# Kernel tuning notes

Hardware: AMD Instinct MI355X
Metric: run time of the kernel (lower is better)

The kernel has to match this reference:

```python
import jax, jax.numpy as jnp
import numpy as np

N_QUBITS = 14
LATENT = 14
DEPTH = 4
BATCH = 256
DIM = 1 << N_QUBITS  # 16384 amplitudes

# PennyLane convention: wire 0 is the most-significant bit of the flat state index.
_idx = np.arange(DIM)
_bits = (_idx[None, :] >> (N_QUBITS - 1 - np.arange(N_QUBITS)[:, None])) & 1  # [n_qubits, DIM]
_parity = np.sum(_bits[:-1] * _bits[1:], axis=0) % 2  # adjacent-pair CZ chain parity
CZ_SIGNS = jnp.asarray(1.0 - 2.0 * _parity, dtype=jnp.complex64)  # [DIM]
Z_SIGNS = jnp.asarray(1 - 2 * _bits[:LATENT], dtype=jnp.float32)  # [LATENT, DIM]


def _rx(t):
    c = jnp.cos(0.5 * t) + 0j
    s = -1j * jnp.sin(0.5 * t)
    m = jnp.stack([jnp.stack([c, s], -1), jnp.stack([s, c], -1)], -2)
    return m.astype(jnp.complex64)


def _ry(t):
    c = jnp.cos(0.5 * t)
    s = jnp.sin(0.5 * t)
    m = jnp.stack([jnp.stack([c, -s], -1), jnp.stack([s, c], -1)], -2)
    return m.astype(jnp.complex64)


def _rz(t):
    e = jnp.exp(-0.5j * t.astype(jnp.complex64))
    z = jnp.zeros_like(e)
    m = jnp.stack([jnp.stack([e, z], -1), jnp.stack([z, jnp.conj(e)], -1)], -2)
    return m.astype(jnp.complex64)


def _apply_1q(state, mat, wire):
    # state: [B, DIM]; mat: [2,2] (shared) or [B,2,2] (per-sample)
    B = state.shape[0]
    left = 1 << wire
    right = 1 << (N_QUBITS - wire - 1)
    st = state.reshape(B, left, 2, right)
    if mat.ndim == 3:
        st = jnp.einsum('bij,bajc->baic', mat, st)
    else:
        st = jnp.einsum('ij,bajc->baic', mat, st)
    return st.reshape(B, DIM)


def setup_inputs() -> dict:
    key = jax.random.key(0)
    k1, k2, k3, k4 = jax.random.split(key, 4)
    conditioning = jax.random.normal(k1, (BATCH, LATENT), dtype=jnp.float32)
    lim = 1.0 / np.sqrt(LATENT)
    W_enc = jax.random.uniform(k2, (N_QUBITS, LATENT), jnp.float32, -lim, lim)
    b_enc = jax.random.uniform(k3, (N_QUBITS,), jnp.float32, -lim, lim)
    # TorchLayer default init: U(0, 2*pi)
    weights = jax.random.uniform(k4, (DEPTH, N_QUBITS, 3), jnp.float32, 0.0, 2.0 * np.pi)
    return {"conditioning": conditioning, "W_enc": W_enc, "b_enc": b_enc, "weights": weights}


def reference(conditioning, W_enc, b_enc, weights):
    # encode: Linear + SiLU -> per-wire rotation angles [B, n_qubits]
    emb = conditioning @ W_enc.T + b_enc
    emb = emb * jax.nn.sigmoid(emb)
    B = emb.shape[0]

    state = jnp.zeros((B, DIM), jnp.complex64).at[:, 0].set(1.0)

    # angle encoding: RX(v) then RY(v) on each wire (per-sample gates)
    for w in range(N_QUBITS):
        v = emb[:, w]
        U = jnp.einsum('bij,bjk->bik', _ry(v), _rx(v))  # [B,2,2]
        state = _apply_1q(state, U, w)

    # variational layers: RZ, RX, RY per wire (shared gates), then CZ chain
    for d in range(DEPTH):
        for w in range(N_QUBITS):
            p = weights[d, w]
            U = _ry(p[2]) @ _rx(p[1]) @ _rz(p[0])  # [2,2]
            state = _apply_1q(state, U, w)
        state = state * CZ_SIGNS  # all adjacent CZs fused into one diagonal

    probs = state.real ** 2 + state.imag ** 2  # [B, DIM]
    latent = probs @ Z_SIGNS.T  # <Z_w> for w in range(LATENT) -> [B, LATENT]

    # F.layer_norm over last dim, no affine params
    mu = jnp.mean(latent, axis=-1, keepdims=True)
    var = jnp.var(latent, axis=-1, keepdims=True)
    return (latent - mu) / jnp.sqrt(var + 1e-5)
```

## Files before the change

### kernel.cpp

```cpp
#include <hip/hip_runtime.h>
#include <math.h>

#define NQ    14
#define DIM   16384
#define DEPTH 4

typedef __attribute__((ext_vector_type(2))) float f2;
typedef __attribute__((ext_vector_type(4))) float f4;

__device__ __forceinline__ f2 cmul(f2 a, f2 b) {
    return (f2){a.x*b.x - a.y*b.y, a.x*b.y + a.y*b.x};
}
__device__ __forceinline__ f2 cmac2(f2 x, f2 u, f2 us, f2 y, f2 v, f2 vs) {
    f2 r = x.xx * u;
    r += x.yy * us;
    r += y.xx * v;
    r += y.yy * vs;
    return r;
}

__device__ __forceinline__ int sw(int e) { return e ^ ((e >> 6) & 0xF); }

__device__ __forceinline__ float czsgn(int e) {
    return (__popc(e & (e >> 1)) & 1) ? -1.0f : 1.0f;
}

template<int CTRL>
__device__ __forceinline__ f2 dpp2(f2 v) {
    union U { f2 f; int i[2]; } u, r;
    u.f = v;
    r.i[0] = __builtin_amdgcn_update_dpp(0, u.i[0], CTRL, 0xF, 0xF, true);
    r.i[1] = __builtin_amdgcn_update_dpp(0, u.i[1], CTRL, 0xF, 0xF, true);
    return r.f;
}
__device__ __forceinline__ f2 swzx4(f2 v) {
    union U { f2 f; int i[2]; } u, r;
    u.f = v;
    r.i[0] = __builtin_amdgcn_ds_swizzle(u.i[0], 0x101F);
    r.i[1] = __builtin_amdgcn_ds_swizzle(u.i[1], 0x101F);
    return r.f;
}
template<int XB> __device__ __forceinline__ f2 lxchg(f2 v);
template<> __device__ __forceinline__ f2 lxchg<1>(f2 v) { return dpp2<0xB1>(v); }
template<> __device__ __forceinline__ f2 lxchg<2>(f2 v) { return dpp2<0x4E>(v); }
template<> __device__ __forceinline__ f2 lxchg<4>(f2 v) { return swzx4(v); }
template<> __device__ __forceinline__ f2 lxchg<8>(f2 v) { return dpp2<0x128>(v); }

template<int SWEEP>
__device__ __forceinline__ int emapS(int t, int s, int l) {
    if (SWEEP == 0)
        return (l << 11) | ((t & 15) << 7)
             | (((t >> 6) & 1) << 6) | (((t >> 7) & 1) << 5) | (((t >> 8) & 1) << 4)
             | (((t >> 5) & 1) << 3) | (((t >> 9) & 1) << 2) | (s << 1) | ((t >> 4) & 1);
    return (s << 13) | (((t >> 4) & 63) << 7) | (l << 4) | (t & 15);
}

template<int MASK>
__device__ __forceinline__ void reg_gate(f2 a[8], const f4* G) {
    f4 g0 = G[0], g1 = G[1], g2 = G[2], g3 = G[3];
    #pragma unroll
    for (int l = 0; l < 8; ++l) {
        if (l & MASK) continue;
        const int j = l | MASK;
        f2 x = a[l], y = a[j];
        a[l] = cmac2(x, g0.xy, g0.zw, y, g1.xy, g1.zw);
        a[j] = cmac2(x, g2.xy, g2.zw, y, g3.xy, g3.zw);
    }
}

template<int XB>
__device__ __forceinline__ void lane_gate(f2 a[8], const f4* G, int t) {
    const bool hi = (t & XB) != 0;
    f4 c1 = G[hi ? 3 : 0];
    f4 c2 = G[hi ? 2 : 1];
    #pragma unroll
    for (int l = 0; l < 8; ++l) {
        f2 p = lxchg<XB>(a[l]);
        a[l] = cmac2(a[l], c1.xy, c1.zw, p, c2.xy, c2.zw);
    }
}

template<int SWEEP>
__device__ __forceinline__ void do_sweep(f2* st, const f4 (*gl)[4], int t,
                                         bool mulsign)
{
    constexpr int QB = (SWEEP == 0) ? 0 : 7;
    #pragma unroll 1
    for (int s = 0; s < 2; ++s) {
        f2 a[8];
        #pragma unroll
        for (int l = 0; l < 8; ++l) a[l] = st[sw(emapS<SWEEP>(t, s, l))];
        if (mulsign) {
            #pragma unroll
            for (int l = 0; l < 8; ++l) a[l] *= czsgn(emapS<SWEEP>(t, s, l));
        }
        reg_gate<4>(a, gl[QB + 0]);
        reg_gate<2>(a, gl[QB + 1]);
        reg_gate<1>(a, gl[QB + 2]);
        lane_gate<8>(a, gl[QB + 3], t);
        lane_gate<4>(a, gl[QB + 4], t);
        lane_gate<2>(a, gl[QB + 5], t);
        lane_gate<1>(a, gl[QB + 6], t);
        #pragma unroll
        for (int l = 0; l < 8; ++l) st[sw(emapS<SWEEP>(t, s, l))] = a[l];
    }
}

__device__ __forceinline__ void do_sweep_final(f2* st, const f4 (*gl)[4], int t,
        float& SU, float& A0, float& Q7, float& Q8, float& Q9)
{
    SU = A0 = Q7 = Q8 = Q9 = 0.f;
    #pragma unroll 1
    for (int s = 0; s < 2; ++s) {
        f2 a[8];
        #pragma unroll
        for (int l = 0; l < 8; ++l) a[l] = st[sw(emapS<1>(t, s, l))];
        reg_gate<4>(a, gl[7]);
        reg_gate<2>(a, gl[8]);
        reg_gate<1>(a, gl[9]);
        lane_gate<8>(a, gl[10], t);
        lane_gate<4>(a, gl[11], t);
        lane_gate<2>(a, gl[12], t);
        lane_gate<1>(a, gl[13], t);
        float p0 = a[0].x*a[0].x + a[0].y*a[0].y;
        float p1 = a[1].x*a[1].x + a[1].y*a[1].y;
        float p2 = a[2].x*a[2].x + a[2].y*a[2].y;
        float p3 = a[3].x*a[3].x + a[3].y*a[3].y;
        float p4 = a[4].x*a[4].x + a[4].y*a[4].y;
        float p5 = a[5].x*a[5].x + a[5].y*a[5].y;
        float p6 = a[6].x*a[6].x + a[6].y*a[6].y;
        float p7 = a[7].x*a[7].x + a[7].y*a[7].y;
        float e0 = p0 + p1, e1 = p2 + p3, e2 = p4 + p5, e3 = p6 + p7;
        float G = (e0 + e1) + (e2 + e3);
        SU += G;
        A0 += s ? -G : G;
        Q7 += (e0 + e1) - (e2 + e3);
        Q8 += (e0 - e1) + (e2 - e3);
        Q9 += (p0 - p1) + (p2 - p3) + (p4 - p5) + (p6 - p7);
    }
}

__global__ __launch_bounds__(1024)
void qlg_kernel(const float* __restrict__ cond,
                const float* __restrict__ Wenc,
                const float* __restrict__ benc,
                const float* __restrict__ wts,
                float* __restrict__ out)
{
    __shared__ f2 st[DIM];
    __shared__ f4 gates[DEPTH][NQ][4];
    __shared__ f2 qv[NQ][2];
    __shared__ f2 Phi[128];
    __shared__ f2 Plo[128];
    __shared__ float embS[NQ];
    __shared__ float wred[16][NQ];
    __shared__ float lat[NQ];

    const int b = blockIdx.x;
    const int t = threadIdx.x;

    if (t < NQ) {
        float s = benc[t];
        #pragma unroll
        for (int k = 0; k < NQ; ++k) s += cond[b*NQ + k] * Wenc[t*NQ + k];
        embS[t] = s / (1.0f + __expf(-s));
    }
    if (t >= 64 && t < 64 + DEPTH*NQ) {
        const int gi = t - 64;
        const int d = gi / NQ, w = gi % NQ;
        const float p0 = wts[(d*NQ + w)*3 + 0];
        const float p1 = wts[(d*NQ + w)*3 + 1];
        const float p2 = wts[(d*NQ + w)*3 + 2];
        float s0, c0, s1, c1, s2, c2;
        sincosf(0.5f*p0, &s0, &c0);
        sincosf(0.5f*p1, &s1, &c1);
        sincosf(0.5f*p2, &s2, &c2);
        f2 e0  = (f2){c0, -s0};
        f2 e0c = (f2){c0,  s0};
        f2 is1 = (f2){0.f, -s1};
        f2 m00 = c1 * e0;
        f2 m01 = cmul(is1, e0c);
        f2 m10 = cmul(is1, e0);
        f2 m11 = c1 * e0c;
        f2 u00 = c2*m00 - s2*m10;
        f2 u01 = c2*m01 - s2*m11;
        f2 u10 = s2*m00 + c2*m10;
        f2 u11 = s2*m01 + c2*m11;
        gates[d][w][0] = (f4){u00.x, u00.y, -u00.y, u00.x};
        gates[d][w][1] = (f4){u01.x, u01.y, -u01.y, u01.x};
        gates[d][w][2] = (f4){u10.x, u10.y, -u10.y, u10.x};
        gates[d][w][3] = (f4){u11.x, u11.y, -u11.y, u11.x};
    }
    __syncthreads();

    if (t < NQ) {
        float v = embS[t];
        float s, c;
        sincosf(0.5f*v, &s, &c);
        f2 a0 = (f2){c*c,  s*s};
        f2 a1 = (f2){s*c, -s*c};
        f2 u00 = gates[0][t][0].xy, u01 = gates[0][t][1].xy;
        f2 u10 = gates[0][t][2].xy, u11 = gates[0][t][3].xy;
        qv[t][0] = cmul(u00, a0) + cmul(u01, a1);
        qv[t][1] = cmul(u10, a0) + cmul(u11, a1);
    }
    __syncthreads();

    if (t < 128) {
        f2 p = qv[0][(t >> 6) & 1];
        #pragma unroll
        for (int w = 1; w <= 6; ++w) p = cmul(p, qv[w][(t >> (6 - w)) & 1]);
        Phi[t] = p;
    } else if (t < 256) {
        const int j = t - 128;
        f2 p = qv[7][(j >> 6) & 1];
        #pragma unroll
        for (int w = 8; w <= 13; ++w) p = cmul(p, qv[w][(j >> (13 - w)) & 1]);
        Plo[j] = p;
    }
    __syncthreads();

    #pragma unroll
    for (int l = 0; l < 16; ++l) {
        const int e = (l << 10) | t;
        f2 v = cmul(Phi[e >> 7], Plo[e & 127]);
        st[sw(e)] = v * czsgn(e);
    }
    __syncthreads();

    do_sweep<0>(st, gates[1], t, false); __syncthreads();
    do_sweep<1>(st, gates[1], t, false); __syncthreads();
    do_sweep<0>(st, gates[2], t, true);  __syncthreads();
    do_sweep<1>(st, gates[2], t, false); __syncthreads();
    do_sweep<0>(st, gates[3], t, true);  __syncthreads();
    float SU, A0, Q7, Q8, Q9;
    do_sweep_final(st, gates[3], t, SU, A0, Q7, Q8, Q9);

    {
        const int lane = t & 63, wv = t >> 6;
        #pragma unroll
        for (int w = 0; w < NQ; ++w) {
            float v;
            if      (w == 0) v = A0;
            else if (w == 7) v = Q7;
            else if (w == 8) v = Q8;
            else if (w == 9) v = Q9;
            else if (w <= 6) v = ((t >> (10 - w)) & 1) ? -SU : SU;
            else             v = ((t >> (13 - w)) & 1) ? -SU : SU;
            #pragma unroll
            for (int off = 32; off > 0; off >>= 1) v += __shfl_down(v, off, 64);
            if (lane == 0) wred[wv][w] = v;
        }
    }
    __syncthreads();
    if (t < NQ) {
        float s = 0.f;
        #pragma unroll
        for (int k = 0; k < 16; ++k) s += wred[k][t];
        lat[t] = s;
    }
    __syncthreads();
    if (t < NQ) {
        float mu = 0.f;
        #pragma unroll
        for (int k = 0; k < NQ; ++k) mu += lat[k];
        mu *= (1.0f / NQ);
        float var = 0.f;
        #pragma unroll
        for (int k = 0; k < NQ; ++k) { float dv = lat[k] - mu; var += dv*dv; }
        var *= (1.0f / NQ);
        out[b*NQ + t] = (lat[t] - mu) * rsqrtf(var + 1e-5f);
    }
}

extern "C" void kernel_launch(void* const* d_in, const int* in_sizes, int n_in,
                              void* d_out, int out_size, void* d_ws, size_t ws_size,
                              hipStream_t stream)
{
    (void)n_in; (void)d_ws; (void)ws_size; (void)out_size;
    const float* cond = (const float*)d_in[0];
    const float* Wenc = (const float*)d_in[1];
    const float* benc = (const float*)d_in[2];
    const float* wts  = (const float*)d_in[3];
    float* out = (float*)d_out;
    const int B = in_sizes[0] / NQ;
    qlg_kernel<<<dim3(B), dim3(1024), 0, stream>>>(cond, Wenc, benc, wts, out);
}
```

Measured before the change: 103.7 us.

## Restructure sweeps to 16 amplitudes per thread with swizzle-free shared layout

Each thread now holds 16 amplitudes in registers instead of two passes of 8, so four qubits are handled as register gates per sweep and fewer need lane exchanges. The shared-memory state is laid out in a permuted order so each sweep reads contiguous or strided addresses without the XOR swizzle. The split between the A and B sweeps is rebalanced (8 qubits, then 6), and the CZ sign and final Z-expectation reductions are rewritten for the new index map. The aim is fewer LDS round trips, less index arithmetic and fewer cross-lane shuffles, at the cost of more registers per thread and possible bank conflicts in the strided accesses.

New measurement: 98.46 us. 1.05x faster.

```diff
diff --git a/kernel.cpp b/kernel.cpp
--- a/kernel.cpp
+++ b/kernel.cpp
@@ -19,11 +19,10 @@
     return r;
 }
 
-__device__ __forceinline__ int sw(int e) { return e ^ ((e >> 6) & 0xF); }
-
 __device__ __forceinline__ float czsgn(int e) {
     return (__popc(e & (e >> 1)) & 1) ? -1.0f : 1.0f;
 }
+
 
 template<int CTRL>
 __device__ __forceinline__ f2 dpp2(f2 v) {
@@ -46,20 +45,11 @@
 template<> __device__ __forceinline__ f2 lxchg<4>(f2 v) { return swzx4(v); }
 template<> __device__ __forceinline__ f2 lxchg<8>(f2 v) { return dpp2<0x128>(v); }
 
-template<int SWEEP>
-__device__ __forceinline__ int emapS(int t, int s, int l) {
-    if (SWEEP == 0)
-        return (l << 11) | ((t & 15) << 7)
-             | (((t >> 6) & 1) << 6) | (((t >> 7) & 1) << 5) | (((t >> 8) & 1) << 4)
-             | (((t >> 5) & 1) << 3) | (((t >> 9) & 1) << 2) | (s << 1) | ((t >> 4) & 1);
-    return (s << 13) | (((t >> 4) & 63) << 7) | (l << 4) | (t & 15);
-}
-
 template<int MASK>
-__device__ __forceinline__ void reg_gate(f2 a[8], const f4* G) {
+__device__ __forceinline__ void reg_gate(f2 a[16], const f4* G) {
     f4 g0 = G[0], g1 = G[1], g2 = G[2], g3 = G[3];
     #pragma unroll
-    for (int l = 0; l < 8; ++l) {
+    for (int l = 0; l < 16; ++l) {
         if (l & MASK) continue;
         const int j = l | MASK;
         f2 x = a[l], y = a[j];
@@ -69,74 +59,89 @@
 }
 
 template<int XB>
-__device__ __forceinline__ void lane_gate(f2 a[8], const f4* G, int t) {
+__device__ __forceinline__ void lane_gate(f2 a[16], const f4* G, int t) {
     const bool hi = (t & XB) != 0;
     f4 c1 = G[hi ? 3 : 0];
     f4 c2 = G[hi ? 2 : 1];
     #pragma unroll
-    for (int l = 0; l < 8; ++l) {
+    for (int l = 0; l < 16; ++l) {
         f2 p = lxchg<XB>(a[l]);
         a[l] = cmac2(a[l], c1.xy, c1.zw, p, c2.xy, c2.zw);
     }
 }
 
-template<int SWEEP>
-__device__ __forceinline__ void do_sweep(f2* st, const f4 (*gl)[4], int t,
-                                         bool mulsign)
-{
-    constexpr int QB = (SWEEP == 0) ? 0 : 7;
-    #pragma unroll 1
-    for (int s = 0; s < 2; ++s) {
-        f2 a[8];
-        #pragma unroll
-        for (int l = 0; l < 8; ++l) a[l] = st[sw(emapS<SWEEP>(t, s, l))];
-        if (mulsign) {
-            #pragma unroll
-            for (int l = 0; l < 8; ++l) a[l] *= czsgn(emapS<SWEEP>(t, s, l));
+template<bool MULSIGN>
+__device__ __forceinline__ void sweepA(f2* st, const f4 (*gl)[4], int t)
+{
+    f2 a[16];
+    #pragma unroll
+    for (int l = 0; l < 16; ++l) a[l] = st[t + (l << 10)];
+    if (MULSIGN) {
+        const int T = ((t & 15) << 6) | (t >> 4);
+        const int pT = __popc(T & (T >> 1)) & 1;
+        const float F0 = pT ? -1.f : 1.f;
+        const float F1 = (pT ^ ((t >> 3) & 1)) ? -1.f : 1.f;
+        #pragma unroll
+        for (int l = 0; l < 16; ++l) {
+            float s = (l & 1) ? F1 : F0;
+            if (__popc(l & (l >> 1)) & 1) s = -s;
+            a[l] *= s;
         }
-        reg_gate<4>(a, gl[QB + 0]);
-        reg_gate<2>(a, gl[QB + 1]);
-        reg_gate<1>(a, gl[QB + 2]);
-        lane_gate<8>(a, gl[QB + 3], t);
-        lane_gate<4>(a, gl[QB + 4], t);
-        lane_gate<2>(a, gl[QB + 5], t);
-        lane_gate<1>(a, gl[QB + 6], t);
-        #pragma unroll
-        for (int l = 0; l < 8; ++l) st[sw(emapS<SWEEP>(t, s, l))] = a[l];
-    }
-}
-
-__device__ __forceinline__ void do_sweep_final(f2* st, const f4 (*gl)[4], int t,
-        float& SU, float& A0, float& Q7, float& Q8, float& Q9)
-{
-    SU = A0 = Q7 = Q8 = Q9 = 0.f;
-    #pragma unroll 1
-    for (int s = 0; s < 2; ++s) {
-        f2 a[8];
-        #pragma unroll
-        for (int l = 0; l < 8; ++l) a[l] = st[sw(emapS<1>(t, s, l))];
-        reg_gate<4>(a, gl[7]);
-        reg_gate<2>(a, gl[8]);
-        reg_gate<1>(a, gl[9]);
-        lane_gate<8>(a, gl[10], t);
-        lane_gate<4>(a, gl[11], t);
-        lane_gate<2>(a, gl[12], t);
-        lane_gate<1>(a, gl[13], t);
-        float p0 = a[0].x*a[0].x + a[0].y*a[0].y;
-        float p1 = a[1].x*a[1].x + a[1].y*a[1].y;
-        float p2 = a[2].x*a[2].x + a[2].y*a[2].y;
-        float p3 = a[3].x*a[3].x + a[3].y*a[3].y;
-        float p4 = a[4].x*a[4].x + a[4].y*a[4].y;
-        float p5 = a[5].x*a[5].x + a[5].y*a[5].y;
-        float p6 = a[6].x*a[6].x + a[6].y*a[6].y;
-        float p7 = a[7].x*a[7].x + a[7].y*a[7].y;
-        float e0 = p0 + p1, e1 = p2 + p3, e2 = p4 + p5, e3 = p6 + p7;
-        float G = (e0 + e1) + (e2 + e3);
-        SU += G;
-        A0 += s ? -G : G;
-        Q7 += (e0 + e1) - (e2 + e3);
-        Q8 += (e0 - e1) + (e2 - e3);
-        Q9 += (p0 - p1) + (p2 - p3) + (p4 - p5) + (p6 - p7);
+    }
+    reg_gate<8>(a, gl[0]);
+    reg_gate<4>(a, gl[1]);
+    reg_gate<2>(a, gl[2]);
+    reg_gate<1>(a, gl[3]);
+    lane_gate<8>(a, gl[4], t);
+    lane_gate<4>(a, gl[5], t);
+    lane_gate<2>(a, gl[6], t);
+    lane_gate<1>(a, gl[7], t);
+    #pragma unroll
+    for (int l = 0; l < 16; ++l) st[t + (l << 10)] = a[l];
+}
+
+__device__ __forceinline__ int baseB(int t) {
+    return ((t >> 2) & 15) | ((t & 3) << 4) | ((t >> 6) << 10);
+}
+
+__device__ __forceinline__ void sweepB(f2* st, const f4 (*gl)[4], int t)
+{
+    const int mb = baseB(t);
+    f2 a[16];
+    #pragma unroll
+    for (int l = 0; l < 16; ++l) a[l] = st[mb + (l << 6)];
+    reg_gate<8>(a, gl[8]);
+    reg_gate<4>(a, gl[9]);
+    reg_gate<2>(a, gl[10]);
+    reg_gate<1>(a, gl[11]);
+    lane_gate<2>(a, gl[12], t);
+    lane_gate<1>(a, gl[13], t);
+    #pragma unroll
+    for (int l = 0; l < 16; ++l) st[mb + (l << 6)] = a[l];
+}
+
+__device__ __forceinline__ void sweepB_final(f2* st, const f4 (*gl)[4], int t,
+        float& SU, float& Q8, float& Q9, float& Q10, float& Q11)
+{
+    const int mb = baseB(t);
+    f2 a[16];
+    #pragma unroll
+    for (int l = 0; l < 16; ++l) a[l] = st[mb + (l << 6)];
+    reg_gate<8>(a, gl[8]);
+    reg_gate<4>(a, gl[9]);
+    reg_gate<2>(a, gl[10]);
+    reg_gate<1>(a, gl[11]);
+    lane_gate<2>(a, gl[12], t);
+    lane_gate<1>(a, gl[13], t);
+    SU = Q8 = Q9 = Q10 = Q11 = 0.f;
+    #pragma unroll
+    for (int l = 0; l < 16; ++l) {
+        float p = a[l].x*a[l].x + a[l].y*a[l].y;
+        SU  += p;
+        Q8  += (l & 8) ? -p : p;
+        Q9  += (l & 4) ? -p : p;
+        Q10 += (l & 2) ? -p : p;
+        Q11 += (l & 1) ? -p : p;
     }
 }
 
@@ -222,31 +227,31 @@
 
     #pragma unroll
     for (int l = 0; l < 16; ++l) {
-        const int e = (l << 10) | t;
+        const int e = (l << 10) | ((t & 15) << 6) | (t >> 4);
         f2 v = cmul(Phi[e >> 7], Plo[e & 127]);
-        st[sw(e)] = v * czsgn(e);
-    }
-    __syncthreads();
-
-    do_sweep<0>(st, gates[1], t, false); __syncthreads();
-    do_sweep<1>(st, gates[1], t, false); __syncthreads();
-    do_sweep<0>(st, gates[2], t, true);  __syncthreads();
-    do_sweep<1>(st, gates[2], t, false); __syncthreads();
-    do_sweep<0>(st, gates[3], t, true);  __syncthreads();
-    float SU, A0, Q7, Q8, Q9;
-    do_sweep_final(st, gates[3], t, SU, A0, Q7, Q8, Q9);
+        st[t + (l << 10)] = v * czsgn(e);
+    }
+    __syncthreads();
+
+    sweepA<false>(st, gates[1], t); __syncthreads();
+    sweepB(st, gates[1], t);        __syncthreads();
+    sweepA<true>(st, gates[2], t);  __syncthreads();
+    sweepB(st, gates[2], t);        __syncthreads();
+    sweepA<true>(st, gates[3], t);  __syncthreads();
+    float SU, Q8, Q9, Q10, Q11;
+    sweepB_final(st, gates[3], t, SU, Q8, Q9, Q10, Q11);
 
     {
         const int lane = t & 63, wv = t >> 6;
         #pragma unroll
         for (int w = 0; w < NQ; ++w) {
             float v;
-            if      (w == 0) v = A0;
-            else if (w == 7) v = Q7;
-            else if (w == 8) v = Q8;
-            else if (w == 9) v = Q9;
-            else if (w <= 6) v = ((t >> (10 - w)) & 1) ? -SU : SU;
-            else             v = ((t >> (13 - w)) & 1) ? -SU : SU;
+            if      (w == 8)  v = Q8;
+            else if (w == 9)  v = Q9;
+            else if (w == 10) v = Q10;
+            else if (w == 11) v = Q11;
+            else if (w <= 7)  v = ((t >> (9 - w)) & 1) ? -SU : SU;
+            else              v = ((t >> (13 - w)) & 1) ? -SU : SU;
             #pragma unroll
             for (int off = 32; off > 0; off >>= 1) v += __shfl_down(v, off, 64);
             if (lane == 0) wred[wv][w] = v;
```
